# Optimization experiments

Hardware: AMD Instinct MI355X
Metric: run time of the kernel (lower is better)

The kernel has to match this reference:

```python
import jax, jax.numpy as jnp
import numpy as np

S, H = 8192, 2048


def setup_inputs() -> dict:
    key = jax.random.key(0)
    k1, k2, k3, k4, k5 = jax.random.split(key, 5)
    encoder_outputs = jax.random.normal(k1, (S, 1, H), dtype=jnp.float32)
    hidden = jax.random.normal(k2, (H,), dtype=jnp.float32)
    # nn.Linear(2H, H): weight [H, 2H], bias [H]
    lim = 1.0 / np.sqrt(2 * H)
    W_att = jax.random.uniform(k3, (H, 2 * H), dtype=jnp.float32, minval=-lim, maxval=lim)
    b_att = jax.random.uniform(k4, (H,), dtype=jnp.float32, minval=-lim, maxval=lim)
    w = jax.random.normal(k5, (1, H), dtype=jnp.float32)
    return {"encoder_outputs": encoder_outputs, "hidden": hidden,
            "W_att": W_att, "b_att": b_att, "w": w}


def reference(encoder_outputs, hidden, W_att, b_att, w):
    # Original loops over source_len: score_i = w . (Linear(cat(hidden, enc_i)))
    # Vectorized: build [S, 2H] once, one GEMM, one dot, one softmax.
    enc = encoder_outputs[:, 0, :]                      # [S, H]
    h = jnp.broadcast_to(hidden[None, :], enc.shape)    # [S, H]
    x = jnp.concatenate([h, enc], axis=1)               # [S, 2H]
    res = x @ W_att.T + b_att                           # [S, H]
    scores = res @ w[0]                                 # [S]
    attn = jax.nn.softmax(scores, axis=0)               # softmax over source_len
    return attn[None, None, :]                          # [1, 1, S]
```

## Files before the change

### kernel.cpp

```cpp
#include <hip/hip_runtime.h>
#include <math.h>

#define SS 8192
#define HH 2048
#define NP 4

__device__ float g_v2p[NP][HH];
__device__ float g_sc[SS];

__global__ __launch_bounds__(256) void colsum_kernel(
    const float* __restrict__ W,
    const float* __restrict__ w)
{
    const int t       = threadIdx.x;
    const int colBase = blockIdx.x * 1024;
    const int row0    = blockIdx.y * 16;
    const float4* base =
        (const float4*)(W + (size_t)row0 * (2 * HH) + HH + colBase) + t;

    float4 wv[16];
#pragma unroll
    for (int j = 0; j < 16; ++j)
        wv[j] = base[(size_t)j * ((2 * HH) / 4)];

    float4 acc = {0.f, 0.f, 0.f, 0.f};
#pragma unroll
    for (int j = 0; j < 16; ++j) {
        const float wj = w[row0 + j];
        acc.x += wj * wv[j].x; acc.y += wj * wv[j].y;
        acc.z += wj * wv[j].z; acc.w += wj * wv[j].w;
    }
    float* dst = &g_v2p[blockIdx.y & (NP - 1)][colBase + t * 4];
    atomicAdd(dst + 0, acc.x);
    atomicAdd(dst + 1, acc.y);
    atomicAdd(dst + 2, acc.z);
    atomicAdd(dst + 3, acc.w);
}

__global__ __launch_bounds__(512) void rowdot_kernel(
    const float* __restrict__ enc)
{
    __shared__ float v2s[HH];
    const int t    = threadIdx.x;
    const int wave = t >> 6;
    const int lane = t & 63;
    const int row  = blockIdx.x * 8 + wave;

    const float4* e = (const float4*)(enc + (size_t)row * HH);
    float4 er[8];
#pragma unroll
    for (int i = 0; i < 8; ++i)
        er[i] = e[lane + i * 64];

    {
        float4 s4 = {0.f, 0.f, 0.f, 0.f};
#pragma unroll
        for (int p = 0; p < NP; ++p) {
            float4 a = ((const float4*)g_v2p[p])[t];
            s4.x += a.x; s4.y += a.y; s4.z += a.z; s4.w += a.w;
        }
        ((float4*)v2s)[t] = s4;
    }
    __syncthreads();

    const float4* v4 = (const float4*)v2s;
    float acc = 0.0f;
#pragma unroll
    for (int i = 0; i < 8; ++i) {
        const float4 vf = v4[lane + i * 64];
        acc += er[i].x * vf.x + er[i].y * vf.y
             + er[i].z * vf.z + er[i].w * vf.w;
    }
#pragma unroll
    for (int off = 32; off > 0; off >>= 1)
        acc += __shfl_down(acc, off);
    if (lane == 0) g_sc[row] = acc;
}

__global__ __launch_bounds__(256) void softmax_kernel(
    float* __restrict__ out)
{
    __shared__ float red[4];
    const int t    = threadIdx.x;
    const int lane = t & 63;
    const int wid  = t >> 6;
    const int b    = blockIdx.x;

    if (b < 8)
        ((float4*)g_v2p)[b * 256 + t] = make_float4(0.f, 0.f, 0.f, 0.f);

    float vals[32];
    float m = -INFINITY;
#pragma unroll
    for (int i = 0; i < 32; ++i) {
        vals[i] = g_sc[t + i * 256];
        m = fmaxf(m, vals[i]);
    }
#pragma unroll
    for (int off = 1; off < 64; off <<= 1)
        m = fmaxf(m, __shfl_xor(m, off));
    if (lane == 0) red[wid] = m;
    __syncthreads();
    m = fmaxf(fmaxf(red[0], red[1]), fmaxf(red[2], red[3]));

    float s = 0.0f;
#pragma unroll
    for (int i = 0; i < 32; ++i)
        s += __expf(vals[i] - m);
#pragma unroll
    for (int off = 1; off < 64; off <<= 1)
        s += __shfl_xor(s, off);
    __syncthreads();
    if (lane == 0) red[wid] = s;
    __syncthreads();
    const float inv = 1.0f / (red[0] + red[1] + red[2] + red[3]);

    if (t < 16) {
        const int e = b * 16 + t;
        out[e] = __expf(g_sc[e] - m) * inv;
    }
}

extern "C" void kernel_launch(void* const* d_in, const int* in_sizes, int n_in,
                              void* d_out, int out_size, void* d_ws, size_t ws_size,
                              hipStream_t stream) {
    const float* enc   = (const float*)d_in[0];
    const float* W_att = (const float*)d_in[2];
    const float* w     = (const float*)d_in[4];

    float* out = (float*)d_out;

    hipLaunchKernelGGL(colsum_kernel,  dim3(2, 128), dim3(256), 0, stream,
                       W_att, w);
    hipLaunchKernelGGL(rowdot_kernel,  dim3(1024),   dim3(512), 0, stream,
                       enc);
    hipLaunchKernelGGL(softmax_kernel, dim3(512),    dim3(256), 0, stream,
                       out);
}
```

Baseline: 121.6 us.

## Fuse column-sum and row-dot kernels with ticket-based grid-wide sync

Merges the W column-reduction kernel and the encoder row-dot kernel into one launch. Blocks take tickets from a global counter; the first 256 tickets also compute an 8-row slice of the w·W reduction, and every block spin-waits on a done counter before reading the summed vector. Encoder rows are loaded into registers before the wait, so the enc stream overlaps the W reduction. The softmax kernel is also changed to read scores as float4. The spin-wait relies on the ticket-holding blocks being resident, and the ever-growing ticket counter must be handled correctly across repeated calls.

After: 152.6 us. 1.26x slower.

```diff
diff --git a/kernel.cpp b/kernel.cpp
--- a/kernel.cpp
+++ b/kernel.cpp
@@ -4,62 +4,91 @@
 #define SS 8192
 #define HH 2048
 #define NP 4
+#define NBLK 1024
+#define NTHR 512
+#define NTILE 256
 
+__device__ unsigned g_tkt  = 0;
+__device__ unsigned g_done = 0;
 __device__ float g_v2p[NP][HH];
 __device__ float g_sc[SS];
 
-__global__ __launch_bounds__(256) void colsum_kernel(
+__global__ __launch_bounds__(NTHR) void fused1_kernel(
+    const float* __restrict__ enc,
     const float* __restrict__ W,
     const float* __restrict__ w)
 {
-    const int t       = threadIdx.x;
-    const int colBase = blockIdx.x * 1024;
-    const int row0    = blockIdx.y * 16;
-    const float4* base =
-        (const float4*)(W + (size_t)row0 * (2 * HH) + HH + colBase) + t;
-
-    float4 wv[16];
-#pragma unroll
-    for (int j = 0; j < 16; ++j)
-        wv[j] = base[(size_t)j * ((2 * HH) / 4)];
-
-    float4 acc = {0.f, 0.f, 0.f, 0.f};
-#pragma unroll
-    for (int j = 0; j < 16; ++j) {
-        const float wj = w[row0 + j];
-        acc.x += wj * wv[j].x; acc.y += wj * wv[j].y;
-        acc.z += wj * wv[j].z; acc.w += wj * wv[j].w;
-    }
-    float* dst = &g_v2p[blockIdx.y & (NP - 1)][colBase + t * 4];
-    atomicAdd(dst + 0, acc.x);
-    atomicAdd(dst + 1, acc.y);
-    atomicAdd(dst + 2, acc.z);
-    atomicAdd(dst + 3, acc.w);
-}
-
-__global__ __launch_bounds__(512) void rowdot_kernel(
-    const float* __restrict__ enc)
-{
-    __shared__ float v2s[HH];
+    const int b    = blockIdx.x;
     const int t    = threadIdx.x;
     const int wave = t >> 6;
     const int lane = t & 63;
-    const int row  = blockIdx.x * 8 + wave;
 
+    __shared__ float v2s[HH];
+    __shared__ unsigned sh_tkt;
+
+    if (t == 0)
+        sh_tkt = __hip_atomic_fetch_add(&g_tkt, 1u, __ATOMIC_RELAXED,
+                                        __HIP_MEMORY_SCOPE_AGENT);
+
+    const int row = b * 8 + wave;
     const float4* e = (const float4*)(enc + (size_t)row * HH);
     float4 er[8];
 #pragma unroll
     for (int i = 0; i < 8; ++i)
         er[i] = e[lane + i * 64];
 
-    {
-        float4 s4 = {0.f, 0.f, 0.f, 0.f};
+    __syncthreads();
+    const unsigned tkt    = sh_tkt;
+    const unsigned tile   = tkt % NBLK;
+    const unsigned target = (tkt / NBLK) * NTILE + NTILE;
+
+    if (tile < NTILE) {
+        const int row0 = (int)tile * 8;
+        const float4* wbase =
+            (const float4*)(W + (size_t)row0 * (2 * HH) + HH) + t;
+        float4 wv[8];
 #pragma unroll
-        for (int p = 0; p < NP; ++p) {
-            float4 a = ((const float4*)g_v2p[p])[t];
-            s4.x += a.x; s4.y += a.y; s4.z += a.z; s4.w += a.w;
+        for (int j = 0; j < 8; ++j)
+            wv[j] = wbase[(size_t)j * ((2 * HH) / 4)];
+        float4 acc = {0.f, 0.f, 0.f, 0.f};
+#pragma unroll
+        for (int j = 0; j < 8; ++j) {
+            const float wj = w[row0 + j];
+            acc.x += wj * wv[j].x; acc.y += wj * wv[j].y;
+            acc.z += wj * wv[j].z; acc.w += wj * wv[j].w;
         }
-        ((float4*)v2s)[t] = s4;
+        float* dst = &g_v2p[tile & (NP - 1)][t * 4];
+        atomicAdd(dst + 0, acc.x);
+        atomicAdd(dst + 1, acc.y);
+        atomicAdd(dst + 2, acc.z);
+        atomicAdd(dst + 3, acc.w);
+    }
+
+#pragma unroll
+    for (int i = 0; i < 8; ++i)
+        asm volatile("" :: "v"(er[i].x), "v"(er[i].y),
+                           "v"(er[i].z), "v"(er[i].w));
+
+    __syncthreads();
+    if (t == 0) {
+        if (tile < NTILE)
+            __hip_atomic_fetch_add(&g_done, 1u, __ATOMIC_RELAXED,
+                                   __HIP_MEMORY_SCOPE_AGENT);
+        while (__hip_atomic_load(&g_done, __ATOMIC_RELAXED,
+                                 __HIP_MEMORY_SCOPE_AGENT) < target)
+            __builtin_amdgcn_s_sleep(8);
+    }
+    __syncthreads();
+
+#pragma unroll
+    for (int k = 0; k < 4; ++k) {
+        const int c = t + k * 512;
+        float s = 0.0f;
+#pragma unroll
+        for (int p = 0; p < NP; ++p)
+            s += __hip_atomic_load(&g_v2p[p][c], __ATOMIC_RELAXED,
+                                   __HIP_MEMORY_SCOPE_AGENT);
+        v2s[c] = s;
     }
     __syncthreads();
 
@@ -89,13 +118,15 @@
     if (b < 8)
         ((float4*)g_v2p)[b * 256 + t] = make_float4(0.f, 0.f, 0.f, 0.f);
 
-    float vals[32];
+    float4 vq[8];
+#pragma unroll
+    for (int i = 0; i < 8; ++i)
+        vq[i] = ((const float4*)g_sc)[t + i * 256];
+
     float m = -INFINITY;
 #pragma unroll
-    for (int i = 0; i < 32; ++i) {
-        vals[i] = g_sc[t + i * 256];
-        m = fmaxf(m, vals[i]);
-    }
+    for (int i = 0; i < 8; ++i)
+        m = fmaxf(fmaxf(fmaxf(m, vq[i].x), fmaxf(vq[i].y, vq[i].z)), vq[i].w);
 #pragma unroll
     for (int off = 1; off < 64; off <<= 1)
         m = fmaxf(m, __shfl_xor(m, off));
@@ -105,8 +136,9 @@
 
     float s = 0.0f;
 #pragma unroll
-    for (int i = 0; i < 32; ++i)
-        s += __expf(vals[i] - m);
+    for (int i = 0; i < 8; ++i)
+        s += __expf(vq[i].x - m) + __expf(vq[i].y - m)
+           + __expf(vq[i].z - m) + __expf(vq[i].w - m);
 #pragma unroll
     for (int off = 1; off < 64; off <<= 1)
         s += __shfl_xor(s, off);
@@ -130,10 +162,8 @@
 
     float* out = (float*)d_out;
 
-    hipLaunchKernelGGL(colsum_kernel,  dim3(2, 128), dim3(256), 0, stream,
-                       W_att, w);
-    hipLaunchKernelGGL(rowdot_kernel,  dim3(1024),   dim3(512), 0, stream,
-                       enc);
-    hipLaunchKernelGGL(softmax_kernel, dim3(512),    dim3(256), 0, stream,
+    hipLaunchKernelGGL(fused1_kernel,  dim3(NBLK), dim3(NTHR), 0, stream,
+                       enc, W_att, w);
+    hipLaunchKernelGGL(softmax_kernel, dim3(512),  dim3(256),  0, stream,
                        out);
 }
```
